# Kernel tuning notes

Measured on AMD Instinct MI355X. Metric: run time of the kernel, lower is better.

The kernel has to match this reference:

```python
import jax, jax.numpy as jnp
import numpy as np

B, CIN, H, W = 4, 128, 256, 256
CH = 96
N = H * W


def _grid_edges(h, w):
    # 4-connected grid, both directions (matches the module's maze_edges lists)
    idx = np.arange(h * w, dtype=np.int32).reshape(h, w)
    l, r = idx[:, :-1].ravel(), idx[:, 1:].ravel()
    u, d = idx[:-1, :].ravel(), idx[1:, :].ravel()
    src = np.concatenate([l, r, u, d])
    dst = np.concatenate([r, l, d, u])
    return np.stack([src, dst])  # [2, E]


def setup_inputs() -> dict:
    key = jax.random.key(0)
    k1, k2, k3 = jax.random.split(key, 3)
    glorot1 = (6.0 / (CIN + CH)) ** 0.5
    glorot2 = (6.0 / (CH + CH)) ** 0.5
    return {
        "x": jax.random.normal(k1, (B, CIN, H, W), dtype=jnp.float32),
        "edge_index": jnp.asarray(_grid_edges(H, W)),
        "W1": jax.random.uniform(k2, (CIN, CH), jnp.float32, -glorot1, glorot1),
        "b1": jnp.zeros((CH,), jnp.float32),
        "W2": jax.random.uniform(k3, (CH, CH), jnp.float32, -glorot2, glorot2),
        "b2": jnp.zeros((CH,), jnp.float32),
    }


def _gcn_conv(h, Wt, b, src, dst, enorm, snorm, n):
    # h: [B, N, Cin] -> PyG GCNConv: D^{-1/2}(A+I)D^{-1/2} (h W) + b
    h = h @ Wt                                   # [B, N, Co]
    msg = h[:, src, :] * enorm[None, :, None]    # gather + edge norm
    agg = jax.vmap(lambda m: jax.ops.segment_sum(m, dst, num_segments=n))(msg)
    return agg + snorm[None, :, None] * h + b    # self-loop term + bias


def reference(x, edge_index, W1, b1, W2, b2):
    b_, c, hgt, wid = x.shape
    n = hgt * wid
    src, dst = edge_index[0], edge_index[1]
    # degrees with self-loops
    deg = jax.ops.segment_sum(jnp.ones_like(src, dtype=x.dtype), dst, num_segments=n) + 1.0
    dinv = jax.lax.rsqrt(deg)
    enorm = dinv[src] * dinv[dst]  # per-edge norm
    snorm = 1.0 / deg              # self-loop norm
    xf = x.reshape(b_, c, n).transpose(0, 2, 1)  # [B, N, C]
    h = jax.nn.relu(_gcn_conv(xf, W1, b1, src, dst, enorm, snorm, n))
    out = _gcn_conv(h, W2, b2, src, dst, enorm, snorm, n)
    return out  # [B, N, CH]
```

## Files before the change

### kernel.cpp

```cpp
#include <hip/hip_runtime.h>
#include <hip/hip_bf16.h>


#define Nn  65536
#define Bb  4

typedef __attribute__((ext_vector_type(8))) short short8;
typedef __attribute__((ext_vector_type(4))) float float4v;

__device__ __forceinline__ float dinv_at(int i, int j) {
    int deg = 1 + (i > 0) + (i < 255) + (j > 0) + (j < 255);
    return rsqrtf((float)deg);
}
__device__ __forceinline__ unsigned short f2bf(float f) {
    __hip_bfloat16 h = __float2bfloat16(f);
    return *reinterpret_cast<unsigned short*>(&h);
}
__device__ __forceinline__ float bf2f(unsigned short u) {
    return __uint_as_float(((unsigned)u) << 16);
}

__global__ void conv_w(const float* __restrict__ W1, const float* __restrict__ W2,
                       unsigned short* __restrict__ wt1, unsigned short* __restrict__ wt2) {
    int t = blockIdx.x * 256 + threadIdx.x;
    if (t < 128 * 96) { int k = t / 96, c = t - k * 96; wt1[c * 128 + k] = f2bf(W1[t]); }
    if (t < 96 * 96)  { int k = t / 96, c = t - k * 96; wt2[c * 96  + k] = f2bf(W2[t]); }
}

template <int K, int NCHUNK, bool FIRST>
__global__ __launch_bounds__(512, 4) void gcn_mfma(
    const void* __restrict__ inp,
    const unsigned short* __restrict__ wtg,
    const float* __restrict__ bias,
    void* __restrict__ outp)
{
    constexpr int SPITCH = 268;
    __shared__ unsigned int sdm[2][16 * SPITCH];

    const int t = threadIdx.x, w = t >> 6, l = t & 63;
    const int wm = w & 3;
    const int cout0 = (w >> 2) * 48;

    const int n_  = blockIdx.x;
    const int xcd = n_ & 7;
    const int p_  = n_ >> 3;
    const int rl  = p_ & 15;
    const int g_  = p_ >> 4;
    const int b   = g_ & 3;
    const int row = (g_ >> 2) * 128 + xcd * 16 + rl;
    const int n0 = row << 8;

    const float dI  = dinv_at(row, 1);
    const float dE  = dinv_at(row, 0);
    const float dUi = (row > 0)   ? dinv_at(row - 1, 1) : 0.f;
    const float dUe = (row > 0)   ? dinv_at(row - 1, 0) : 0.f;
    const float dDi = (row < 255) ? dinv_at(row + 1, 1) : 0.f;
    const float dDe = (row < 255) ? dinv_at(row + 1, 0) : 0.f;

    const int  lj = FIRST ? l : (l & 31);
    const bool eL = (lj == 0), eR = (lj == (FIRST ? 63 : 31));
    const float dC0 = eL ? dE : dI, dU0 = eL ? dUe : dUi, dD0 = eL ? dDe : dDi;
    const float dL0 = eL ? 0.f : dI;
    const float dL1 = eL ? dE  : dI;
    const float dRm = eR ? dE  : dI;
    const float dCl = eR ? dE : dI, dUl = eR ? dUe : dUi, dDl = eR ? dDe : dDi;
    const float dRl = eR ? 0.f : dI;

    const int rup = (row > 0)   ? -256 : 0;
    const int rdn = (row < 255) ?  256 : 0;

    float4v acc[12];
#pragma unroll
    for (int q_ = 0; q_ < 12; ++q_) acc[q_] = (float4v){0.f, 0.f, 0.f, 0.f};

    const size_t ibase = (size_t)b * K * Nn + n0;
    const int q = l >> 4, m = l & 15;

    short8 wf[3];

    for (int ch = 0; ch < NCHUNK; ++ch) {
        unsigned int* sb = sdm[ch & 1];

#pragma unroll
        for (int mt = 0; mt < 3; ++mt)
            wf[mt] = *(const short8*)&wtg[(size_t)(cout0 + mt * 16 + m) * K + ch * 32 + q * 8];

        if (FIRST) {
            const float* xp = (const float*)inp;
#pragma unroll
            for (int p = 0; p < 2; ++p) {
                const int kp = w * 2 + p;
                float y[2][4];
#pragma unroll
                for (int par = 0; par < 2; ++par) {
                    const int k = ch * 32 + kp * 2 + par;
                    const float* pl = xp + ibase + (size_t)k * Nn + 4 * l;
                    const float4 c = *(const float4*)pl;
                    const float4 u = *(const float4*)(pl + rup);
                    const float4 d = *(const float4*)(pl + rdn);
                    const float lm = __shfl_up(c.w, 1);
                    const float rp = __shfl_down(c.x, 1);
                    y[par][0] = dC0 * (dC0 * c.x + dL0 * lm  + dI  * c.y + dU0 * u.x + dD0 * d.x);
                    y[par][1] = dI  * (dI  * c.y + dL1 * c.x + dI  * c.z + dUi * u.y + dDi * d.y);
                    y[par][2] = dI  * (dI  * c.z + dI  * c.y + dRm * c.w + dUi * u.z + dDi * d.z);
                    y[par][3] = dCl * (dCl * c.w + dI  * c.z + dRl * rp  + dUl * u.w + dDl * d.w);
                }
                unsigned pk[4];
#pragma unroll
                for (int tn = 0; tn < 4; ++tn)
                    pk[tn] = (unsigned)f2bf(y[0][tn]) | ((unsigned)f2bf(y[1][tn]) << 16);
                *(short8*)&sb[kp * SPITCH + 4 * l] = *(short8*)pk;
            }
        } else {
            const unsigned short* hp = (const unsigned short*)inp;
#pragma unroll
            for (int p = 0; p < 2; ++p) {
                const int kp = w * 2 + p;
                const int k = ch * 32 + kp * 2 + (l >> 5);
                const unsigned short* pl = hp + ibase + (size_t)k * Nn + 8 * (l & 31);
                const short8 c8 = *(const short8*)pl;
                const short8 u8 = *(const short8*)(pl + rup);
                const short8 d8 = *(const short8*)(pl + rdn);
                float cc[8], uu[8], dd[8];
#pragma unroll
                for (int tn = 0; tn < 8; ++tn) {
                    cc[tn] = bf2f((unsigned short)c8[tn]);
                    uu[tn] = bf2f((unsigned short)u8[tn]);
                    dd[tn] = bf2f((unsigned short)d8[tn]);
                }
                const float lm = bf2f((unsigned short)__shfl_up((int)(unsigned short)c8[7], 1));
                const float rp = bf2f((unsigned short)__shfl_down((int)(unsigned short)c8[0], 1));
                float y[8];
                y[0] = dC0 * (dC0 * cc[0] + dL0 * lm    + dI  * cc[1] + dU0 * uu[0] + dD0 * dd[0]);
                y[1] = dI  * (dI  * cc[1] + dL1 * cc[0] + dI  * cc[2] + dUi * uu[1] + dDi * dd[1]);
#pragma unroll
                for (int tn = 2; tn < 6; ++tn)
                    y[tn] = dI * (dI * (cc[tn - 1] + cc[tn] + cc[tn + 1]) + dUi * uu[tn] + dDi * dd[tn]);
                y[6] = dI  * (dI  * cc[6] + dI  * cc[5] + dRm * cc[7] + dUi * uu[6] + dDi * dd[6]);
                y[7] = dCl * (dCl * cc[7] + dI  * cc[6] + dRl * rp    + dUl * uu[7] + dDl * dd[7]);
                unsigned pk[8];
#pragma unroll
                for (int tn = 0; tn < 8; ++tn) {
                    const float hi = __shfl(y[tn], (l & 31) + 32);
                    pk[tn] = (unsigned)f2bf(y[tn]) | ((unsigned)f2bf(hi) << 16);
                }
                if (l < 32) {
                    *(short8*)&sb[kp * SPITCH + 8 * (l & 31)]     = *(short8*)&pk[0];
                    *(short8*)&sb[kp * SPITCH + 8 * (l & 31) + 4] = *(short8*)&pk[4];
                }
            }
        }

        asm volatile("s_waitcnt lgkmcnt(0)" ::: "memory");
        __builtin_amdgcn_s_barrier();
        asm volatile("" ::: "memory");
        __builtin_amdgcn_sched_barrier(0);

#pragma unroll
        for (int ct = 0; ct < 4; ++ct) {
            const int nodem = (wm * 4 + ct) * 16 + m;
            union { unsigned u4[4]; short8 s; } df;
#pragma unroll
            for (int jj = 0; jj < 4; ++jj)
                df.u4[jj] = sb[(q * 4 + jj) * SPITCH + nodem];
#pragma unroll
            for (int mt = 0; mt < 3; ++mt) {
                if (FIRST)
                    acc[ct * 3 + mt] = __builtin_amdgcn_mfma_f32_16x16x32_bf16(
                        wf[mt], df.s, acc[ct * 3 + mt], 0, 0, 0);
                else
                    acc[ct * 3 + mt] = __builtin_amdgcn_mfma_f32_16x16x32_bf16(
                        df.s, wf[mt], acc[ct * 3 + mt], 0, 0, 0);
            }
        }
    }

    if (FIRST) {
        unsigned short* hb = (unsigned short*)outp + (size_t)b * 96 * Nn + n0;
#pragma unroll
        for (int ct = 0; ct < 4; ++ct) {
            const int node = (wm * 4 + ct) * 16 + m;
#pragma unroll
            for (int mt = 0; mt < 3; ++mt)
#pragma unroll
                for (int r = 0; r < 4; ++r) {
                    const int cout = cout0 + mt * 16 + q * 4 + r;
                    const float v = acc[ct * 3 + mt][r] + bias[cout];
                    hb[(size_t)cout * Nn + node] = f2bf(fmaxf(v, 0.f));
                }
        }
    } else {
        float* ob = (float*)outp + ((size_t)b * Nn + n0) * 96;
#pragma unroll
        for (int nt = 0; nt < 4; ++nt)
#pragma unroll
            for (int mt = 0; mt < 3; ++mt) {
                const int cout = cout0 + mt * 16 + m;
                const float bv = bias[cout];
#pragma unroll
                for (int r = 0; r < 4; ++r) {
                    const int node = (wm * 4 + nt) * 16 + q * 4 + r;
                    ob[(size_t)node * 96 + cout] = acc[nt * 3 + mt][r] + bv;
                }
            }
    }
}

extern "C" void kernel_launch(void* const* d_in, const int* in_sizes, int n_in,
                              void* d_out, int out_size, void* d_ws, size_t ws_size,
                              hipStream_t stream) {
    const float* x  = (const float*)d_in[0];
    const float* W1 = (const float*)d_in[2];
    const float* b1 = (const float*)d_in[3];
    const float* W2 = (const float*)d_in[4];
    const float* b2 = (const float*)d_in[5];
    float* out = (float*)d_out;

    unsigned short* h   = (unsigned short*)d_ws;
    unsigned short* wt1 = (unsigned short*)((char*)d_ws + 50331648);
    unsigned short* wt2 = (unsigned short*)((char*)d_ws + 50331648 + 24576);

    conv_w<<<48, 256, 0, stream>>>(W1, W2, wt1, wt2);
    gcn_mfma<128, 4, true ><<<1024, 512, 0, stream>>>(x, wt1, b1, h);
    gcn_mfma< 96, 3, false><<<1024, 512, 0, stream>>>(h, wt2, b2, out);
}
```

Before: 276.4 us.

## Split stencil aggregation out of GEMM kernels into separate bf16 stencil passes

Instead of applying the normalized 4-neighbour stencil inside each MFMA GEMM kernel, layer 1 now does the GEMM first on raw x (computing XW before aggregation), then runs standalone stencil kernels for the layer-1 aggregation with bias+ReLU and the layer-2 aggregation before the second GEMM. This removes the up/down neighbour reads of fp32 x, which tripled input traffic in the first kernel, and the shuffle-heavy packing in the GEMM loaders. The cost is two extra launches and extra round trips of 96-channel bf16 intermediates through global memory, plus an extra workspace buffer.

Result: slower. 294.1 us (+6.4%).

```diff
diff --git a/kernel.cpp b/kernel.cpp
--- a/kernel.cpp
+++ b/kernel.cpp
@@ -6,6 +6,7 @@
 #define Bb  4
 
 typedef __attribute__((ext_vector_type(8))) short short8;
+typedef __attribute__((ext_vector_type(4))) short short4v;
 typedef __attribute__((ext_vector_type(4))) float float4v;
 
 __device__ __forceinline__ float dinv_at(int i, int j) {
@@ -27,8 +28,73 @@
     if (t < 96 * 96)  { int k = t / 96, c = t - k * 96; wt2[c * 96  + k] = f2bf(W2[t]); }
 }
 
-template <int K, int NCHUNK, bool FIRST>
-__global__ __launch_bounds__(512, 4) void gcn_mfma(
+template <bool FIN>
+__global__ __launch_bounds__(256, 8) void gcn_sten(
+    const unsigned short* __restrict__ inp,
+    const float* __restrict__ bias,
+    unsigned short* __restrict__ outp)
+{
+    const int t = threadIdx.x, w = t >> 6, l = t & 63;
+    const int bi = blockIdx.x;
+    const int rb = bi & 31;
+    const int pc = bi >> 5;
+    const int row = rb * 8 + w * 2 + (l >> 5);
+    const int lj = l & 31;
+
+    const float dI  = dinv_at(row, 1);
+    const float dE  = dinv_at(row, 0);
+    const float dUi = (row > 0)   ? dinv_at(row - 1, 1) : 0.f;
+    const float dUe = (row > 0)   ? dinv_at(row - 1, 0) : 0.f;
+    const float dDi = (row < 255) ? dinv_at(row + 1, 1) : 0.f;
+    const float dDe = (row < 255) ? dinv_at(row + 1, 0) : 0.f;
+    const bool eL = (lj == 0), eR = (lj == 31);
+    const float dC0 = eL ? dE : dI, dU0 = eL ? dUe : dUi, dD0 = eL ? dDe : dDi;
+    const float dL0 = eL ? 0.f : dI;
+    const float dL1 = eL ? dE  : dI;
+    const float dRm = eR ? dE  : dI;
+    const float dCl = eR ? dE : dI, dUl = eR ? dUe : dUi, dDl = eR ? dDe : dDi;
+    const float dRl = eR ? 0.f : dI;
+
+    const int rup = (row > 0)   ? -256 : 0;
+    const int rdn = (row < 255) ?  256 : 0;
+
+    const size_t off = (size_t)pc * Nn + row * 256 + lj * 8;
+    const unsigned short* pl = inp + off;
+    const short8 c8 = *(const short8*)pl;
+    const short8 u8 = *(const short8*)(pl + rup);
+    const short8 d8 = *(const short8*)(pl + rdn);
+    float cc[8], uu[8], dd[8];
+#pragma unroll
+    for (int tn = 0; tn < 8; ++tn) {
+        cc[tn] = bf2f((unsigned short)c8[tn]);
+        uu[tn] = bf2f((unsigned short)u8[tn]);
+        dd[tn] = bf2f((unsigned short)d8[tn]);
+    }
+    const float lm = bf2f((unsigned short)__shfl_up((int)(unsigned short)c8[7], 1));
+    const float rp = bf2f((unsigned short)__shfl_down((int)(unsigned short)c8[0], 1));
+    float y[8];
+    y[0] = dC0 * (dC0 * cc[0] + dL0 * lm    + dI  * cc[1] + dU0 * uu[0] + dD0 * dd[0]);
+    y[1] = dI  * (dI  * cc[1] + dL1 * cc[0] + dI  * cc[2] + dUi * uu[1] + dDi * dd[1]);
+#pragma unroll
+    for (int tn = 2; tn < 6; ++tn)
+        y[tn] = dI * (dI * (cc[tn - 1] + cc[tn] + cc[tn + 1]) + dUi * uu[tn] + dDi * dd[tn]);
+    y[6] = dI  * (dI  * cc[6] + dI  * cc[5] + dRm * cc[7] + dUi * uu[6] + dDi * dd[6]);
+    y[7] = dCl * (dCl * cc[7] + dI  * cc[6] + dRl * rp    + dUl * uu[7] + dDl * dd[7]);
+
+    float bv = 0.f;
+    if constexpr (FIN) { const int c = pc - (pc / 96) * 96; bv = bias[c]; }
+    short8 ov;
+#pragma unroll
+    for (int tn = 0; tn < 8; ++tn) {
+        float v = y[tn] + bv;
+        if constexpr (FIN) v = fmaxf(v, 0.f);
+        ov[tn] = (short)f2bf(v);
+    }
+    *(short8*)(outp + off) = ov;
+}
+
+template <int K, int NCHUNK, bool L1G>
+__global__ __launch_bounds__(512, 4) void gcn_gemm(
     const void* __restrict__ inp,
     const unsigned short* __restrict__ wtg,
     const float* __restrict__ bias,
@@ -50,25 +116,6 @@
     const int row = (g_ >> 2) * 128 + xcd * 16 + rl;
     const int n0 = row << 8;
 
-    const float dI  = dinv_at(row, 1);
-    const float dE  = dinv_at(row, 0);
-    const float dUi = (row > 0)   ? dinv_at(row - 1, 1) : 0.f;
-    const float dUe = (row > 0)   ? dinv_at(row - 1, 0) : 0.f;
-    const float dDi = (row < 255) ? dinv_at(row + 1, 1) : 0.f;
-    const float dDe = (row < 255) ? dinv_at(row + 1, 0) : 0.f;
-
-    const int  lj = FIRST ? l : (l & 31);
-    const bool eL = (lj == 0), eR = (lj == (FIRST ? 63 : 31));
-    const float dC0 = eL ? dE : dI, dU0 = eL ? dUe : dUi, dD0 = eL ? dDe : dDi;
-    const float dL0 = eL ? 0.f : dI;
-    const float dL1 = eL ? dE  : dI;
-    const float dRm = eR ? dE  : dI;
-    const float dCl = eR ? dE : dI, dUl = eR ? dUe : dUi, dDl = eR ? dDe : dDi;
-    const float dRl = eR ? 0.f : dI;
-
-    const int rup = (row > 0)   ? -256 : 0;
-    const int rdn = (row < 255) ?  256 : 0;
-
     float4v acc[12];
 #pragma unroll
     for (int q_ = 0; q_ < 12; ++q_) acc[q_] = (float4v){0.f, 0.f, 0.f, 0.f};
@@ -85,30 +132,22 @@
         for (int mt = 0; mt < 3; ++mt)
             wf[mt] = *(const short8*)&wtg[(size_t)(cout0 + mt * 16 + m) * K + ch * 32 + q * 8];
 
-        if (FIRST) {
+        if (L1G) {
             const float* xp = (const float*)inp;
 #pragma unroll
             for (int p = 0; p < 2; ++p) {
                 const int kp = w * 2 + p;
-                float y[2][4];
-#pragma unroll
-                for (int par = 0; par < 2; ++par) {
-                    const int k = ch * 32 + kp * 2 + par;
-                    const float* pl = xp + ibase + (size_t)k * Nn + 4 * l;
-                    const float4 c = *(const float4*)pl;
-                    const float4 u = *(const float4*)(pl + rup);
-                    const float4 d = *(const float4*)(pl + rdn);
-                    const float lm = __shfl_up(c.w, 1);
-                    const float rp = __shfl_down(c.x, 1);
-                    y[par][0] = dC0 * (dC0 * c.x + dL0 * lm  + dI  * c.y + dU0 * u.x + dD0 * d.x);
-                    y[par][1] = dI  * (dI  * c.y + dL1 * c.x + dI  * c.z + dUi * u.y + dDi * d.y);
-                    y[par][2] = dI  * (dI  * c.z + dI  * c.y + dRm * c.w + dUi * u.z + dDi * d.z);
-                    y[par][3] = dCl * (dCl * c.w + dI  * c.z + dRl * rp  + dUl * u.w + dDl * d.w);
-                }
+                const int k = ch * 32 + kp * 2;
+                const float* p0 = xp + ibase + (size_t)k * Nn + 4 * l;
+                const float* p1 = p0 + Nn;
+                const float4 a0 = *(const float4*)p0;
+                const float4 a1 = *(const float4*)p1;
+                const float e0[4] = {a0.x, a0.y, a0.z, a0.w};
+                const float e1[4] = {a1.x, a1.y, a1.z, a1.w};
                 unsigned pk[4];
 #pragma unroll
                 for (int tn = 0; tn < 4; ++tn)
-                    pk[tn] = (unsigned)f2bf(y[0][tn]) | ((unsigned)f2bf(y[1][tn]) << 16);
+                    pk[tn] = (unsigned)f2bf(e0[tn]) | ((unsigned)f2bf(e1[tn]) << 16);
                 *(short8*)&sb[kp * SPITCH + 4 * l] = *(short8*)pk;
             }
         } else {
@@ -116,38 +155,16 @@
 #pragma unroll
             for (int p = 0; p < 2; ++p) {
                 const int kp = w * 2 + p;
-                const int k = ch * 32 + kp * 2 + (l >> 5);
-                const unsigned short* pl = hp + ibase + (size_t)k * Nn + 8 * (l & 31);
-                const short8 c8 = *(const short8*)pl;
-                const short8 u8 = *(const short8*)(pl + rup);
-                const short8 d8 = *(const short8*)(pl + rdn);
-                float cc[8], uu[8], dd[8];
-#pragma unroll
-                for (int tn = 0; tn < 8; ++tn) {
-                    cc[tn] = bf2f((unsigned short)c8[tn]);
-                    uu[tn] = bf2f((unsigned short)u8[tn]);
-                    dd[tn] = bf2f((unsigned short)d8[tn]);
-                }
-                const float lm = bf2f((unsigned short)__shfl_up((int)(unsigned short)c8[7], 1));
-                const float rp = bf2f((unsigned short)__shfl_down((int)(unsigned short)c8[0], 1));
-                float y[8];
-                y[0] = dC0 * (dC0 * cc[0] + dL0 * lm    + dI  * cc[1] + dU0 * uu[0] + dD0 * dd[0]);
-                y[1] = dI  * (dI  * cc[1] + dL1 * cc[0] + dI  * cc[2] + dUi * uu[1] + dDi * dd[1]);
-#pragma unroll
-                for (int tn = 2; tn < 6; ++tn)
-                    y[tn] = dI * (dI * (cc[tn - 1] + cc[tn] + cc[tn + 1]) + dUi * uu[tn] + dDi * dd[tn]);
-                y[6] = dI  * (dI  * cc[6] + dI  * cc[5] + dRm * cc[7] + dUi * uu[6] + dDi * dd[6]);
-                y[7] = dCl * (dCl * cc[7] + dI  * cc[6] + dRl * rp    + dUl * uu[7] + dDl * dd[7]);
-                unsigned pk[8];
-#pragma unroll
-                for (int tn = 0; tn < 8; ++tn) {
-                    const float hi = __shfl(y[tn], (l & 31) + 32);
-                    pk[tn] = (unsigned)f2bf(y[tn]) | ((unsigned)f2bf(hi) << 16);
-                }
-                if (l < 32) {
-                    *(short8*)&sb[kp * SPITCH + 8 * (l & 31)]     = *(short8*)&pk[0];
-                    *(short8*)&sb[kp * SPITCH + 8 * (l & 31) + 4] = *(short8*)&pk[4];
-                }
+                const int k = ch * 32 + kp * 2;
+                const unsigned short* p0 = hp + ibase + (size_t)k * Nn + 4 * l;
+                const short4v e = *(const short4v*)p0;
+                const short4v o = *(const short4v*)(p0 + Nn);
+                unsigned pk[4];
+#pragma unroll
+                for (int tn = 0; tn < 4; ++tn)
+                    pk[tn] = (unsigned)(unsigned short)e[tn]
+                           | ((unsigned)(unsigned short)o[tn] << 16);
+                *(short8*)&sb[kp * SPITCH + 4 * l] = *(short8*)pk;
             }
         }
 
@@ -165,7 +182,7 @@
                 df.u4[jj] = sb[(q * 4 + jj) * SPITCH + nodem];
 #pragma unroll
             for (int mt = 0; mt < 3; ++mt) {
-                if (FIRST)
+                if (L1G)
                     acc[ct * 3 + mt] = __builtin_amdgcn_mfma_f32_16x16x32_bf16(
                         wf[mt], df.s, acc[ct * 3 + mt], 0, 0, 0);
                 else
@@ -175,7 +192,7 @@
         }
     }
 
-    if (FIRST) {
+    if (L1G) {
         unsigned short* hb = (unsigned short*)outp + (size_t)b * 96 * Nn + n0;
 #pragma unroll
         for (int ct = 0; ct < 4; ++ct) {
@@ -185,8 +202,7 @@
 #pragma unroll
                 for (int r = 0; r < 4; ++r) {
                     const int cout = cout0 + mt * 16 + q * 4 + r;
-                    const float v = acc[ct * 3 + mt][r] + bias[cout];
-                    hb[(size_t)cout * Nn + node] = f2bf(fmaxf(v, 0.f));
+                    hb[(size_t)cout * Nn + node] = f2bf(acc[ct * 3 + mt][r]);
                 }
         }
     } else {
@@ -216,11 +232,14 @@
     const float* b2 = (const float*)d_in[5];
     float* out = (float*)d_out;
 
-    unsigned short* h   = (unsigned short*)d_ws;
-    unsigned short* wt1 = (unsigned short*)((char*)d_ws + 50331648);
-    unsigned short* wt2 = (unsigned short*)((char*)d_ws + 50331648 + 24576);
+    unsigned short* y   = (unsigned short*)d_ws;
+    unsigned short* h   = (unsigned short*)((char*)d_ws + 50331648);
+    unsigned short* wt1 = (unsigned short*)((char*)d_ws + 100663296);
+    unsigned short* wt2 = (unsigned short*)((char*)d_ws + 100663296 + 24576);
 
     conv_w<<<48, 256, 0, stream>>>(W1, W2, wt1, wt2);
-    gcn_mfma<128, 4, true ><<<1024, 512, 0, stream>>>(x, wt1, b1, h);
-    gcn_mfma< 96, 3, false><<<1024, 512, 0, stream>>>(h, wt2, b2, out);
-}
+    gcn_gemm<128, 4, true ><<<1024, 512, 0, stream>>>(x, wt1, nullptr, y);
+    gcn_sten<true ><<<12288, 256, 0, stream>>>(y, b1, h);
+    gcn_sten<false><<<12288, 256, 0, stream>>>(h, nullptr, y);
+    gcn_gemm< 96, 3, false><<<1024, 512, 0, stream>>>(y, wt2, b2, out);
+}
```
